# Kernel tuning notes

Measured on AMD Instinct MI355X. Metric: run time of the kernel, lower is better.

## Reference

```python
import jax, jax.numpy as jnp
import numpy as np


def _encode(tab, idx):
    # tab: [F, V, D]; idx: [..., F] int -> sum_f tab[f, idx[..., f]] -> [..., D]
    g = jax.vmap(lambda t, i: t[i], in_axes=(0, -1), out_axes=0)(tab, idx)
    return g.sum(0)


def _diffuse(fea, ei, w, order):
    # fea: [N, D]; ei: [2, E]; w: [E] learned edge weights
    N = fea.shape[0]
    r, c = ei[0], ei[1]
    adj = jnp.zeros((N, N), fea.dtype).at[r, c].set(w).at[c, r].set(w)
    adj = adj + jnp.eye(N, dtype=fea.dtype)
    r_col_inv = adj.sum(1) ** -0.5  # from degree over axis 1
    r_row_inv = adj.sum(0) ** -0.5  # from degree over axis 0
    A = r_row_inv[:, None] * adj * r_col_inv[None, :]
    x = fea
    y = fea
    for _ in range(order):
        x = jax.lax.stop_gradient(A @ x)
        y = y + x
    return jax.lax.stop_gradient(y / (order + 1.0))


def setup_inputs():
    B, N, E, EMB, L, FA, FB, V = 512, 128, 512, 300, 5, 9, 3, 64
    k = jax.random.split(jax.random.key(0), 12)
    s = 0.02
    return {
        "order": 3,
        "x_atom": jax.random.randint(k[0], (B, N, FA), 0, V),
        "edge_index": jax.random.randint(k[1], (B, 2, E), 0, N),
        "edge_attr": jax.random.randint(k[2], (B, E, FB), 0, V),
        "atom_tab": jax.random.normal(k[3], (FA, V, EMB)) * s,
        "bond_tab_root": jax.random.normal(k[4], (FB, V, EMB)) * s,
        "edge_lin_w": jax.random.normal(k[5], (EMB,)) * s,
        "edge_lin_b": jnp.zeros(()),
        "bond_tabs": jax.random.normal(k[6], (L, FB, V, EMB)) * s,
        "eps": jnp.zeros((L,)),
        "w1": jax.random.normal(k[7], (L, EMB, 2 * EMB)) * s,
        "b1": jnp.zeros((L, 2 * EMB)),
        "bn1_g": jnp.ones((L, 2 * EMB)),
        "bn1_b": jnp.zeros((L, 2 * EMB)),
        "w2": jax.random.normal(k[8], (L, 2 * EMB, EMB)) * s,
        "b2": jnp.zeros((L, EMB)),
        "bn_g": jnp.ones((L, EMB)),
        "bn_b": jnp.zeros((L, EMB)),
    }


def reference(order, x_atom, edge_index, edge_attr, atom_tab, bond_tab_root,
              edge_lin_w, edge_lin_b, bond_tabs, eps, w1, b1, bn1_g, bn1_b,
              w2, b2, bn_g, bn_b):
    B, N = x_atom.shape[:2]
    E = edge_index.shape[-1]
    L = w1.shape[0]
    DROP = 0.2  # node-feature drop rate (eval-mode scaling)

    # --- per-graph dense-adjacency diffusion (vmapped over graphs) ---
    fea = _encode(atom_tab, x_atom) * (1.0 - DROP)                 # [B, N, D]
    e_emb = _encode(bond_tab_root, edge_attr)                      # [B, E, D]
    ew = jax.nn.sigmoid(e_emb @ edge_lin_w + edge_lin_b)           # [B, E]
    h = jax.vmap(_diffuse, in_axes=(0, 0, 0, None))(fea, edge_index, ew, order)
    h = h.reshape(B * N, -1)                                       # [B*N, D]

    # --- globally-batched GIN message passing ---
    off = (jnp.arange(B) * N)[:, None]
    src = (edge_index[:, 0, :] + off).reshape(-1)                  # [B*E]
    dst = (edge_index[:, 1, :] + off).reshape(-1)
    ea_flat = edge_attr.reshape(B * E, -1)

    for l in range(L):
        ee = _encode(bond_tabs[l], ea_flat)                        # [B*E, D]
        msg = jax.nn.relu(h[src] + ee)
        agg = jax.ops.segment_sum(msg, dst, num_segments=B * N)
        z = (1.0 + eps[l]) * h + agg
        z = z @ w1[l] + b1[l]
        z = bn1_g[l] * z + bn1_b[l]   # eval-mode BN (running mean 0, var 1)
        z = jax.nn.relu(z)
        z = z @ w2[l] + b2[l]
        z = bn_g[l] * z + bn_b[l]     # outer eval-mode BN
        if l < L - 1:
            z = jax.nn.relu(z)
        h = z
    return h
```

## Files before the change

kernel.cpp:

```cpp
#include <hip/hip_runtime.h>

#define NGRAPH 512
#define NNODE  128
#define NEDGE  512
#define EMB    300
#define NLAYER 5
#define FA     9
#define FB     3
#define VV     64
#define KPAD   136

typedef __bf16 bf16x8 __attribute__((ext_vector_type(8)));
typedef __bf16 bf16x4 __attribute__((ext_vector_type(4)));
typedef float  f32x4  __attribute__((ext_vector_type(4)));

__device__ __forceinline__ void gload_lds16(const void* gptr, void* lptr) {
    __builtin_amdgcn_global_load_lds(
        (const __attribute__((address_space(1))) void*)gptr,
        (__attribute__((address_space(3))) void*)lptr, 16, 0, 0);
}

__global__ __launch_bounds__(256)
void prep_w_kernel(const float* __restrict__ w1, const float* __restrict__ w2,
                   __bf16* __restrict__ w1t, __bf16* __restrict__ w2t)
{
    const int i = blockIdx.x * 256 + threadIdx.x;
    const int T1 = NLAYER * 640 * 320;
    const int T2 = NLAYER * 320 * 640;
    if (i < T1) {
        const int l = i / (640 * 320);
        const int r = i - l * 640 * 320;
        const int n = r / 320, k = r - n * 320;
        float v = (n < 600 && k < 300) ? w1[((size_t)l * 300 + k) * 600 + n] : 0.f;
        w1t[i] = (__bf16)v;
    } else if (i < T1 + T2) {
        const int j = i - T1;
        const int l = j / (320 * 640);
        const int r = j - l * 320 * 640;
        const int n = r / 640, k = r - n * 640;
        float v = (n < 300 && k < 600) ? w2[((size_t)l * 600 + k) * 300 + n] : 0.f;
        w2t[j] = (__bf16)v;
    }
}

__global__ __launch_bounds__(512)
void adj_kernel(const int* __restrict__ edge_index,
                const int* __restrict__ edge_attr,
                const float* __restrict__ bond_tab_root,
                const float* __restrict__ edge_lin_w,
                const float* __restrict__ edge_lin_b,
                __bf16* __restrict__ Ahi_g, __bf16* __restrict__ Alo_g)
{
    __shared__ float A[128 * 129];
    __shared__ float ew_s[NEDGE];
    __shared__ int   es[NEDGE];
    __shared__ float rinv[128];
    __shared__ float cinv[128];

    const int tid = threadIdx.x;
    const int g   = blockIdx.x;
    int* Ai = (int*)A;

    for (int e = tid; e < NEDGE; e += 512) {
        int r = edge_index[(g * 2 + 0) * NEDGE + e];
        int c = edge_index[(g * 2 + 1) * NEDGE + e];
        es[e] = r | (c << 8);
    }
    for (int i = tid; i < 128 * 129; i += 512) Ai[i] = -1;
    __syncthreads();

    {
        const int wave = tid >> 6, lane = tid & 63;
        const float elb = edge_lin_b[0];
        for (int e = wave * 64; e < wave * 64 + 64; ++e) {
            const int base = (g * NEDGE + e) * 3;
            const int a0 = edge_attr[base + 0];
            const int a1 = edge_attr[base + 1];
            const int a2 = edge_attr[base + 2];
            const float* t0 = bond_tab_root + (0 * VV + a0) * EMB;
            const float* t1 = bond_tab_root + (1 * VV + a1) * EMB;
            const float* t2 = bond_tab_root + (2 * VV + a2) * EMB;
            float acc = 0.f;
            for (int d = lane; d < EMB; d += 64)
                acc += (t0[d] + t1[d] + t2[d]) * edge_lin_w[d];
            #pragma unroll
            for (int off = 32; off > 0; off >>= 1) acc += __shfl_xor(acc, off, 64);
            if (lane == 0) ew_s[e] = 1.f / (1.f + expf(-(acc + elb)));
        }
    }
    for (int e = tid; e < NEDGE; e += 512) {
        int r = es[e] & 255, c = es[e] >> 8;
        atomicMax(&Ai[r * 129 + c], e);
        atomicMax(&Ai[c * 129 + r], 512 + e);
    }
    __syncthreads();
    for (int i = tid; i < 128 * 129; i += 512) {
        int p = Ai[i];
        A[i] = (p < 0) ? 0.f : ew_s[p & 511];
    }
    __syncthreads();
    if (tid < 128) A[tid * 129 + tid] += 1.f;
    __syncthreads();
    if (tid < 128) {
        float rs = 0.f, cs = 0.f;
        for (int j = 0; j < 128; ++j) { rs += A[tid * 129 + j]; cs += A[j * 129 + tid]; }
        rinv[tid] = 1.f / sqrtf(rs);
        cinv[tid] = 1.f / sqrtf(cs);
    }
    __syncthreads();
    for (int i = tid; i < 128 * KPAD; i += 512) {
        const int m = i / KPAD, k = i - m * KPAD;
        float v = (k < 128) ? A[m * 129 + k] * cinv[m] * rinv[k] : 0.f;
        __bf16 hi = (__bf16)v;
        Ahi_g[(size_t)g * 128 * KPAD + i] = hi;
        Alo_g[(size_t)g * 128 * KPAD + i] = (__bf16)(v - (float)hi);
    }
}

__global__ __launch_bounds__(512)
void diffuse_mm_kernel(const int* __restrict__ order_p,
                       const int* __restrict__ x_atom,
                       const float* __restrict__ atom_tab,
                       const __bf16* __restrict__ Ahi_g,
                       const __bf16* __restrict__ Alo_g,
                       float* __restrict__ h)
{
    __shared__ __bf16 Ahi[128 * KPAD];
    __shared__ __bf16 Alo[128 * KPAD];
    __shared__ __bf16 xt[4 * 64 * KPAD];
    __shared__ int    xat[128 * FA];

    const int tid  = threadIdx.x;
    const int g    = blockIdx.x;
    const int lane = tid & 63;
    const int wid  = tid >> 6;
    const int wm   = (wid >> 1) * 32;
    const int wn   = (wid & 1) * 32;
    const int lr   = lane & 15;
    const int q4   = (lane >> 4) * 4;
    const int kc   = (lane >> 4) * 8;

    for (int idx = tid; idx < 128 * KPAD / 8; idx += 512) {
        gload_lds16(Ahi_g + (size_t)g * 128 * KPAD + idx * 8, (char*)Ahi + idx * 16);
        gload_lds16(Alo_g + (size_t)g * 128 * KPAD + idx * 8, (char*)Alo + idx * 16);
    }
    for (int i = tid; i < 128 * FA; i += 512) xat[i] = x_atom[g * 128 * FA + i];
    __syncthreads();

    const int   ord    = order_p[0];
    const float yscale = 1.f / (float)(ord + 1);

    for (int cb = 0; cb < 5; ++cb) {
        const int dbase = cb * 64;

        float yacc[2][2][4];
        #pragma unroll
        for (int mi = 0; mi < 2; ++mi) {
            #pragma unroll
            for (int ni = 0; ni < 2; ++ni) {
                const int n_ = wn + ni * 16 + lr;
                const int d  = dbase + n_;
                #pragma unroll
                for (int r = 0; r < 4; ++r) {
                    const int m_ = wm + mi * 16 + q4 + r;
                    float v = 0.f;
                    if (d < EMB) {
                        #pragma unroll
                        for (int f = 0; f < FA; ++f)
                            v += atom_tab[(size_t)((f << 6) + xat[m_ * FA + f]) * EMB + d];
                        v *= 0.8f;
                    }
                    yacc[mi][ni][r] = v;
                    __bf16 hi = (__bf16)v;
                    xt[0 * 64 * KPAD + n_ * KPAD + m_] = hi;
                    xt[1 * 64 * KPAD + n_ * KPAD + m_] = (__bf16)(v - (float)hi);
                }
            }
        }
        __syncthreads();

        int curbuf = 0;
        for (int o = 0; o < ord; ++o) {
            const __bf16* xh = xt + (curbuf * 2 + 0) * 64 * KPAD;
            const __bf16* xl = xt + (curbuf * 2 + 1) * 64 * KPAD;
            f32x4 racc[2][2];
            #pragma unroll
            for (int mi = 0; mi < 2; ++mi)
                #pragma unroll
                for (int ni = 0; ni < 2; ++ni) racc[mi][ni] = (f32x4){0.f, 0.f, 0.f, 0.f};

            #pragma unroll
            for (int ks = 0; ks < 4; ++ks) {
                const int k0 = ks * 32 + kc;
                bf16x8 ah[2], al[2], bh[2], bl[2];
                #pragma unroll
                for (int mi = 0; mi < 2; ++mi) {
                    ah[mi] = *(const bf16x8*)&Ahi[(wm + mi * 16 + lr) * KPAD + k0];
                    al[mi] = *(const bf16x8*)&Alo[(wm + mi * 16 + lr) * KPAD + k0];
                }
                #pragma unroll
                for (int ni = 0; ni < 2; ++ni) {
                    bh[ni] = *(const bf16x8*)&xh[(wn + ni * 16 + lr) * KPAD + k0];
                    bl[ni] = *(const bf16x8*)&xl[(wn + ni * 16 + lr) * KPAD + k0];
                }
                #pragma unroll
                for (int mi = 0; mi < 2; ++mi) {
                    #pragma unroll
                    for (int ni = 0; ni < 2; ++ni) {
                        racc[mi][ni] = __builtin_amdgcn_mfma_f32_16x16x32_bf16(
                            ah[mi], bh[ni], racc[mi][ni], 0, 0, 0);
                        racc[mi][ni] = __builtin_amdgcn_mfma_f32_16x16x32_bf16(
                            ah[mi], bl[ni], racc[mi][ni], 0, 0, 0);
                        racc[mi][ni] = __builtin_amdgcn_mfma_f32_16x16x32_bf16(
                            al[mi], bh[ni], racc[mi][ni], 0, 0, 0);
                    }
                }
            }

            __bf16* nh = xt + ((curbuf ^ 1) * 2 + 0) * 64 * KPAD;
            __bf16* nl = xt + ((curbuf ^ 1) * 2 + 1) * 64 * KPAD;
            #pragma unroll
            for (int mi = 0; mi < 2; ++mi) {
                #pragma unroll
                for (int ni = 0; ni < 2; ++ni) {
                    const int n_ = wn + ni * 16 + lr;
                    const int mbase = wm + mi * 16 + q4;
                    bf16x4 hv, lv;
                    #pragma unroll
                    for (int r = 0; r < 4; ++r) {
                        const float v = racc[mi][ni][r];
                        yacc[mi][ni][r] += v;
                        __bf16 hi = (__bf16)v;
                        hv[r] = hi;
                        lv[r] = (__bf16)(v - (float)hi);
                    }
                    *(bf16x4*)&nh[n_ * KPAD + mbase] = hv;
                    *(bf16x4*)&nl[n_ * KPAD + mbase] = lv;
                }
            }
            __syncthreads();
            curbuf ^= 1;
        }

        #pragma unroll
        for (int mi = 0; mi < 2; ++mi) {
            #pragma unroll
            for (int ni = 0; ni < 2; ++ni) {
                const int n_ = wn + ni * 16 + lr;
                const int d  = dbase + n_;
                if (d < EMB) {
                    #pragma unroll
                    for (int r = 0; r < 4; ++r) {
                        const int m_ = wm + mi * 16 + q4 + r;
                        h[(size_t)(g * 128 + m_) * EMB + d] = yacc[mi][ni][r] * yscale;
                    }
                }
            }
        }
    }
}

__global__ __launch_bounds__(1024)
void agg_kernel(const int* __restrict__ edge_index,
                const int* __restrict__ edge_attr,
                const float* __restrict__ bond_tabs,
                const float* __restrict__ eps_all,
                const int l,
                const float* __restrict__ h,
                __bf16* __restrict__ zb)
{
    __shared__ __bf16         hs[128 * 160];
    __shared__ int            epk[NEDGE];
    __shared__ unsigned short eord[NEDGE];
    __shared__ int            cnt[128];
    __shared__ int            off_[129];
    __shared__ int            fill[128];

    const int tid  = threadIdx.x;
    const int g    = blockIdx.x >> 1;
    const int coff = (blockIdx.x & 1) * 160;
    const int wave = tid >> 6, lane = tid & 63;
    const float epl = 1.f + eps_all[l];
    const float* bt = bond_tabs + (size_t)l * FB * VV * EMB;

    if (tid < 128) { cnt[tid] = 0; fill[tid] = 0; }
    __syncthreads();
    if (tid < NEDGE) {
        const int s_ = edge_index[(g * 2 + 0) * NEDGE + tid];
        const int d_ = edge_index[(g * 2 + 1) * NEDGE + tid];
        const int base = (g * NEDGE + tid) * 3;
        epk[tid] = s_ | (d_ << 7) | (edge_attr[base + 0] << 14)
                 | (edge_attr[base + 1] << 20) | (edge_attr[base + 2] << 26);
        atomicAdd(&cnt[d_], 1);
    }
    for (int idx = tid; idx < 128 * 40; idx += 1024) {
        const int r = idx / 40, q = (idx - r * 40) * 4;
        bf16x4 v;
        #pragma unroll
        for (int j = 0; j < 4; ++j) {
            const int d = coff + q + j;
            v[j] = (__bf16)((d < EMB) ? h[(size_t)(g * 128 + r) * EMB + d] : 0.f);
        }
        *(bf16x4*)&hs[r * 160 + q] = v;
    }
    __syncthreads();
    if (tid < 64) {
        const int a = cnt[tid];
        const int b = cnt[64 + tid];
        int ia = a;
        #pragma unroll
        for (int o = 1; o < 64; o <<= 1) {
            int t = __shfl_up(ia, o, 64);
            if (tid >= o) ia += t;
        }
        const int totA = __shfl(ia, 63, 64);
        int ib = b;
        #pragma unroll
        for (int o = 1; o < 64; o <<= 1) {
            int t = __shfl_up(ib, o, 64);
            if (tid >= o) ib += t;
        }
        off_[tid]      = ia - a;
        off_[64 + tid] = totA + ib - b;
        if (tid == 63) off_[128] = totA + ib;
    }
    __syncthreads();
    if (tid < NEDGE) {
        const int d_ = (epk[tid] >> 7) & 127;
        const int pos = off_[d_] + atomicAdd(&fill[d_], 1);
        eord[pos] = (unsigned short)tid;
    }
    __syncthreads();

    const int d0 = lane, d1 = lane + 64, d2 = lane + 128;
    const bool r0 = (coff + d0) < EMB;
    const bool r1 = (coff + d1) < EMB;
    const bool r2 = (d2 < 160) && ((coff + d2) < EMB);

    for (int n = wave; n < 128; n += 16) {
        const float* hrow = h + (size_t)(g * 128 + n) * EMB + coff;
        float a0 = r0 ? epl * hrow[d0] : 0.f;
        float a1 = r1 ? epl * hrow[d1] : 0.f;
        float a2 = r2 ? epl * hrow[d2] : 0.f;
        const int eEnd = off_[n + 1];
        for (int ee = off_[n]; ee < eEnd; ++ee) {
            const int p   = epk[eord[ee]];
            const int src = p & 127;
            const float* t0 = bt + ((p >> 14) & 63) * EMB + coff;
            const float* t1 = bt + (64  + ((p >> 20) & 63)) * EMB + coff;
            const float* t2 = bt + (128 + ((p >> 26) & 63)) * EMB + coff;
            if (r0) a0 += fmaxf((float)hs[src * 160 + d0] + t0[d0] + t1[d0] + t2[d0], 0.f);
            if (r1) a1 += fmaxf((float)hs[src * 160 + d1] + t0[d1] + t1[d1] + t2[d1], 0.f);
            if (r2) a2 += fmaxf((float)hs[src * 160 + d2] + t0[d2] + t1[d2] + t2[d2], 0.f);
        }
        __bf16* zrow = zb + (size_t)(g * 128 + n) * 320 + coff;
        zrow[d0] = (__bf16)a0;
        zrow[d1] = (__bf16)a1;
        if (d2 < 160) zrow[d2] = (__bf16)a2;
    }
}

template <int ABF16, int CBF16, int RELU>
__global__ __launch_bounds__(256)
void gemm_mfma(const void* __restrict__ Av, const int lda, const int Kreal,
               const int nT, const int nBlkN, const __bf16* __restrict__ B,
               void* __restrict__ Cv, const int ldc, const int Nreal,
               const float* __restrict__ bias, const float* __restrict__ gam,
               const float* __restrict__ bet)
{
    __shared__ unsigned short As[128 * 32];
    __shared__ unsigned short Bs[64 * 32];

    const int tid  = threadIdx.x;
    const int nwg  = gridDim.x;
    const int hw   = blockIdx.x;
    const int lg   = (hw & 7) * (nwg >> 3) + (hw >> 3);
    const int bn   = (lg % nBlkN) * 64;
    const int bm   = (lg / nBlkN) * 128;
    const int wid  = tid >> 6;
    const int lane = tid & 63;
    const int wm   = (wid >> 1) * 64;
    const int wn   = (wid & 1) * 32;
    const int lr   = lane & 15;
    const int kc   = (lane >> 4) * 8;
    const int KP   = nT * 32;

    f32x4 acc[4][2];
    #pragma unroll
    for (int mi = 0; mi < 4; ++mi)
        #pragma unroll
        for (int ni = 0; ni < 2; ++ni) acc[mi][ni] = (f32x4){0.f, 0.f, 0.f, 0.f};

    for (int t = 0; t < nT; ++t) {
        const int k0 = t * 32;
        {
            const int n = tid >> 2, k8 = (tid & 3) * 8;
            gload_lds16(B + (size_t)(bn + n) * KP + k0 + k8,
                        (char*)Bs + tid * 16);
        }
        if (ABF16) {
            const __bf16* A = (const __bf16*)Av;
            #pragma unroll
            for (int q = 0; q < 2; ++q) {
                const int idx = q * 256 + tid;
                const int m = idx >> 2, k8 = (idx & 3) * 8;
                gload_lds16(A + (size_t)(bm + m) * lda + k0 + k8,
                            (char*)As + idx * 16);
            }
        } else {
            const float* A = (const float*)Av;
            #pragma unroll
            for (int q = 0; q < 2; ++q) {
                const int idx = q * 256 + tid;
                const int m = idx >> 2;
                const int k = k0 + (idx & 3) * 8;
                const float* src = A + (size_t)(bm + m) * lda + k;
                float v[8];
                if (k + 7 < Kreal) {
                    const float4 u0 = *(const float4*)src;
                    const float4 u1 = *(const float4*)(src + 4);
                    v[0] = u0.x; v[1] = u0.y; v[2] = u0.z; v[3] = u0.w;
                    v[4] = u1.x; v[5] = u1.y; v[6] = u1.z; v[7] = u1.w;
                } else {
                    #pragma unroll
                    for (int j = 0; j < 8; ++j) v[j] = (k + j < Kreal) ? src[j] : 0.f;
                }
                bf16x8 p;
                #pragma unroll
                for (int j = 0; j < 8; ++j) p[j] = (__bf16)v[j];
                *(bf16x8*)&As[idx * 8] = p;
            }
        }
        __syncthreads();

        bf16x8 a[4], bfr[2];
        #pragma unroll
        for (int mi = 0; mi < 4; ++mi)
            a[mi] = *(const bf16x8*)&As[(wm + mi * 16 + lr) * 32 + kc];
        #pragma unroll
        for (int ni = 0; ni < 2; ++ni)
            bfr[ni] = *(const bf16x8*)&Bs[(wn + ni * 16 + lr) * 32 + kc];
        #pragma unroll
        for (int mi = 0; mi < 4; ++mi)
            #pragma unroll
            for (int ni = 0; ni < 2; ++ni)
                acc[mi][ni] = __builtin_amdgcn_mfma_f32_16x16x32_bf16(
                    a[mi], bfr[ni], acc[mi][ni], 0, 0, 0);
        __syncthreads();
    }

    #pragma unroll
    for (int ni = 0; ni < 2; ++ni) {
        const int n = bn + wn + ni * 16 + lr;
        const bool nv = (n < Nreal);
        const float gv = nv ? gam[n]  : 0.f;
        const float bv = nv ? bias[n] : 0.f;
        const float ev = nv ? bet[n]  : 0.f;
        #pragma unroll
        for (int mi = 0; mi < 4; ++mi) {
            #pragma unroll
            for (int r = 0; r < 4; ++r) {
                const size_t m = bm + wm + mi * 16 + (lane >> 4) * 4 + r;
                float v = gv * (acc[mi][ni][r] + bv) + ev;
                if (RELU) v = fmaxf(v, 0.f);
                if (CBF16) {
                    ((__bf16*)Cv)[m * ldc + n] = (__bf16)v;
                } else if (nv) {
                    ((float*)Cv)[m * ldc + n] = v;
                }
            }
        }
    }
}

extern "C" void kernel_launch(void* const* d_in, const int* in_sizes, int n_in,
                              void* d_out, int out_size, void* d_ws, size_t ws_size,
                              hipStream_t stream)
{
    const int*   order_p       = (const int*)d_in[0];
    const int*   x_atom        = (const int*)d_in[1];
    const int*   edge_index    = (const int*)d_in[2];
    const int*   edge_attr     = (const int*)d_in[3];
    const float* atom_tab      = (const float*)d_in[4];
    const float* bond_tab_root = (const float*)d_in[5];
    const float* edge_lin_w    = (const float*)d_in[6];
    const float* edge_lin_b    = (const float*)d_in[7];
    const float* bond_tabs     = (const float*)d_in[8];
    const float* eps           = (const float*)d_in[9];
    const float* w1            = (const float*)d_in[10];
    const float* b1            = (const float*)d_in[11];
    const float* bn1g          = (const float*)d_in[12];
    const float* bn1b          = (const float*)d_in[13];
    const float* w2            = (const float*)d_in[14];
    const float* b2            = (const float*)d_in[15];
    const float* bng           = (const float*)d_in[16];
    const float* bnb           = (const float*)d_in[17];

    float* h = (float*)d_out;

    char* ws = (char*)d_ws;
    __bf16* Ahi_g = (__bf16*)ws;
    __bf16* Alo_g = (__bf16*)(ws + 17825792);
    __bf16* z1    = (__bf16*)ws;
    __bf16* w1t   = (__bf16*)(ws + 83886080);
    __bf16* w2t   = (__bf16*)(ws + 83886080 + 2048000);
    __bf16* zb    = (__bf16*)(ws + 83886080 + 4096000);

    prep_w_kernel<<<8000, 256, 0, stream>>>(w1, w2, w1t, w2t);

    adj_kernel<<<NGRAPH, 512, 0, stream>>>(edge_index, edge_attr, bond_tab_root,
                                           edge_lin_w, edge_lin_b, Ahi_g, Alo_g);

    diffuse_mm_kernel<<<NGRAPH, 512, 0, stream>>>(order_p, x_atom, atom_tab,
                                                  Ahi_g, Alo_g, h);

    for (int l = 0; l < NLAYER; ++l) {
        agg_kernel<<<NGRAPH * 2, 1024, 0, stream>>>(
            edge_index, edge_attr, bond_tabs, eps, l, h, zb);

        gemm_mfma<1, 1, 1><<<5120, 256, 0, stream>>>(
            zb, 320, 320, 10, 10, w1t + (size_t)l * 640 * 320,
            z1, 640, 600, b1 + l * 600, bn1g + l * 600, bn1b + l * 600);

        if (l < NLAYER - 1) {
            gemm_mfma<1, 0, 1><<<2560, 256, 0, stream>>>(
                z1, 640, 640, 20, 5, w2t + (size_t)l * 320 * 640,
                h, EMB, 300, b2 + l * 300, bng + l * 300, bnb + l * 300);
        } else {
            gemm_mfma<1, 0, 0><<<2560, 256, 0, stream>>>(
                z1, 640, 640, 20, 5, w2t + (size_t)l * 320 * 640,
                h, EMB, 300, b2 + l * 300, bng + l * 300, bnb + l * 300);
        }
    }
}
```

Baseline: 1.176 ms.

## Precompute per-graph CSR once and keep intermediate node features in padded bf16

Adds a csr_kernel that builds the destination-sorted packed edge list and offsets once per graph, so the five agg_kernel launches no longer rebuild them with atomics and scans each layer. The diffusion output and the intermediate second-GEMM outputs are now stored as bf16 rows padded to 320 in the output buffer, and agg loads them with vector copies instead of converting from fp32. This halves the node-feature traffic and removes per-layer setup. It adds one extra launch, and the csr kernel's serial scan over 512 edges per thread is slow but runs only once.

Measured after the change: 1.097 ms. 6.7% less time.

```diff
diff --git a/kernel.cpp b/kernel.cpp
--- a/kernel.cpp
+++ b/kernel.cpp
@@ -43,6 +43,60 @@
     }
 }
 
+__global__ __launch_bounds__(128)
+void csr_kernel(const int* __restrict__ edge_index,
+                const int* __restrict__ edge_attr,
+                int* __restrict__ epk_sorted,
+                int* __restrict__ off_g)
+{
+    __shared__ int epk_s[NEDGE];
+    __shared__ int cnt[128];
+    __shared__ int off_[129];
+
+    const int tid = threadIdx.x;
+    const int g   = blockIdx.x;
+
+    cnt[tid] = 0;
+    __syncthreads();
+    for (int e = tid; e < NEDGE; e += 128) {
+        const int s_ = edge_index[(g * 2 + 0) * NEDGE + e];
+        const int d_ = edge_index[(g * 2 + 1) * NEDGE + e];
+        const int base = (g * NEDGE + e) * 3;
+        epk_s[e] = s_ | (d_ << 7) | (edge_attr[base + 0] << 14)
+                 | (edge_attr[base + 1] << 20) | (edge_attr[base + 2] << 26);
+        atomicAdd(&cnt[d_], 1);
+    }
+    __syncthreads();
+    if (tid < 64) {
+        const int a = cnt[tid];
+        const int b = cnt[64 + tid];
+        int ia = a;
+        #pragma unroll
+        for (int o = 1; o < 64; o <<= 1) {
+            int t = __shfl_up(ia, o, 64);
+            if (tid >= o) ia += t;
+        }
+        const int totA = __shfl(ia, 63, 64);
+        int ib = b;
+        #pragma unroll
+        for (int o = 1; o < 64; o <<= 1) {
+            int t = __shfl_up(ib, o, 64);
+            if (tid >= o) ib += t;
+        }
+        off_[tid]      = ia - a;
+        off_[64 + tid] = totA + ib - b;
+        if (tid == 63) off_[128] = totA + ib;
+    }
+    __syncthreads();
+    off_g[g * 129 + tid] = off_[tid];
+    if (tid == 0) off_g[g * 129 + 128] = off_[128];
+    int pos = off_[tid];
+    for (int e = 0; e < NEDGE; ++e) {
+        const int p = epk_s[e];
+        if (((p >> 7) & 127) == tid) epk_sorted[(g << 9) + pos++] = p;
+    }
+}
+
 __global__ __launch_bounds__(512)
 void adj_kernel(const int* __restrict__ edge_index,
                 const int* __restrict__ edge_attr,
@@ -123,7 +177,7 @@
                        const float* __restrict__ atom_tab,
                        const __bf16* __restrict__ Ahi_g,
                        const __bf16* __restrict__ Alo_g,
-                       float* __restrict__ h)
+                       __bf16* __restrict__ hb)
 {
     __shared__ __bf16 Ahi[128 * KPAD];
     __shared__ __bf16 Alo[128 * KPAD];
@@ -248,12 +302,11 @@
             for (int ni = 0; ni < 2; ++ni) {
                 const int n_ = wn + ni * 16 + lr;
                 const int d  = dbase + n_;
-                if (d < EMB) {
-                    #pragma unroll
-                    for (int r = 0; r < 4; ++r) {
-                        const int m_ = wm + mi * 16 + q4 + r;
-                        h[(size_t)(g * 128 + m_) * EMB + d] = yacc[mi][ni][r] * yscale;
-                    }
+                #pragma unroll
+                for (int r = 0; r < 4; ++r) {
+                    const int m_ = wm + mi * 16 + q4 + r;
+                    const float v = (d < EMB) ? yacc[mi][ni][r] * yscale : 0.f;
+                    hb[(size_t)(g * 128 + m_) * 320 + d] = (__bf16)v;
                 }
             }
         }
@@ -261,20 +314,15 @@
 }
 
 __global__ __launch_bounds__(1024)
-void agg_kernel(const int* __restrict__ edge_index,
-                const int* __restrict__ edge_attr,
+void agg_kernel(const __bf16* __restrict__ hb,
+                const int* __restrict__ epk_sorted,
+                const int* __restrict__ off_g,
                 const float* __restrict__ bond_tabs,
                 const float* __restrict__ eps_all,
                 const int l,
-                const float* __restrict__ h,
                 __bf16* __restrict__ zb)
 {
-    __shared__ __bf16         hs[128 * 160];
-    __shared__ int            epk[NEDGE];
-    __shared__ unsigned short eord[NEDGE];
-    __shared__ int            cnt[128];
-    __shared__ int            off_[129];
-    __shared__ int            fill[128];
+    __shared__ __bf16 hs[128 * 160];
 
     const int tid  = threadIdx.x;
     const int g    = blockIdx.x >> 1;
@@ -283,52 +331,10 @@
     const float epl = 1.f + eps_all[l];
     const float* bt = bond_tabs + (size_t)l * FB * VV * EMB;
 
-    if (tid < 128) { cnt[tid] = 0; fill[tid] = 0; }
-    __syncthreads();
-    if (tid < NEDGE) {
-        const int s_ = edge_index[(g * 2 + 0) * NEDGE + tid];
-        const int d_ = edge_index[(g * 2 + 1) * NEDGE + tid];
-        const int base = (g * NEDGE + tid) * 3;
-        epk[tid] = s_ | (d_ << 7) | (edge_attr[base + 0] << 14)
-                 | (edge_attr[base + 1] << 20) | (edge_attr[base + 2] << 26);
-        atomicAdd(&cnt[d_], 1);
-    }
-    for (int idx = tid; idx < 128 * 40; idx += 1024) {
-        const int r = idx / 40, q = (idx - r * 40) * 4;
-        bf16x4 v;
-        #pragma unroll
-        for (int j = 0; j < 4; ++j) {
-            const int d = coff + q + j;
-            v[j] = (__bf16)((d < EMB) ? h[(size_t)(g * 128 + r) * EMB + d] : 0.f);
-        }
-        *(bf16x4*)&hs[r * 160 + q] = v;
-    }
-    __syncthreads();
-    if (tid < 64) {
-        const int a = cnt[tid];
-        const int b = cnt[64 + tid];
-        int ia = a;
-        #pragma unroll
-        for (int o = 1; o < 64; o <<= 1) {
-            int t = __shfl_up(ia, o, 64);
-            if (tid >= o) ia += t;
-        }
-        const int totA = __shfl(ia, 63, 64);
-        int ib = b;
-        #pragma unroll
-        for (int o = 1; o < 64; o <<= 1) {
-            int t = __shfl_up(ib, o, 64);
-            if (tid >= o) ib += t;
-        }
-        off_[tid]      = ia - a;
-        off_[64 + tid] = totA + ib - b;
-        if (tid == 63) off_[128] = totA + ib;
-    }
-    __syncthreads();
-    if (tid < NEDGE) {
-        const int d_ = (epk[tid] >> 7) & 127;
-        const int pos = off_[d_] + atomicAdd(&fill[d_], 1);
-        eord[pos] = (unsigned short)tid;
+    for (int idx = tid; idx < 128 * 20; idx += 1024) {
+        const int r = idx / 20, c = idx - r * 20;
+        *(bf16x8*)&hs[r * 160 + c * 8] =
+            *(const bf16x8*)&hb[(size_t)(g * 128 + r) * 320 + coff + c * 8];
     }
     __syncthreads();
 
@@ -337,14 +343,16 @@
     const bool r1 = (coff + d1) < EMB;
     const bool r2 = (d2 < 160) && ((coff + d2) < EMB);
 
+    const int* offg = off_g + g * 129;
+    const int* epkg = epk_sorted + (g << 9);
+
     for (int n = wave; n < 128; n += 16) {
-        const float* hrow = h + (size_t)(g * 128 + n) * EMB + coff;
-        float a0 = r0 ? epl * hrow[d0] : 0.f;
-        float a1 = r1 ? epl * hrow[d1] : 0.f;
-        float a2 = r2 ? epl * hrow[d2] : 0.f;
-        const int eEnd = off_[n + 1];
-        for (int ee = off_[n]; ee < eEnd; ++ee) {
-            const int p   = epk[eord[ee]];
+        float a0 = r0 ? epl * (float)hs[n * 160 + d0] : 0.f;
+        float a1 = r1 ? epl * (float)hs[n * 160 + d1] : 0.f;
+        float a2 = r2 ? epl * (float)hs[n * 160 + d2] : 0.f;
+        const int eBeg = offg[n], eEnd = offg[n + 1];
+        for (int ee = eBeg; ee < eEnd; ++ee) {
+            const int p   = epkg[ee];
             const int src = p & 127;
             const float* t0 = bt + ((p >> 14) & 63) * EMB + coff;
             const float* t1 = bt + (64  + ((p >> 20) & 63)) * EMB + coff;
@@ -496,7 +504,8 @@
     const float* bng           = (const float*)d_in[16];
     const float* bnb           = (const float*)d_in[17];
 
-    float* h = (float*)d_out;
+    float*  h  = (float*)d_out;
+    __bf16* hb = (__bf16*)d_out;
 
     char* ws = (char*)d_ws;
     __bf16* Ahi_g = (__bf16*)ws;
@@ -505,27 +514,31 @@
     __bf16* w1t   = (__bf16*)(ws + 83886080);
     __bf16* w2t   = (__bf16*)(ws + 83886080 + 2048000);
     __bf16* zb    = (__bf16*)(ws + 83886080 + 4096000);
+    int*    epk_s = (int*)(ws + 83886080 + 4096000 + 41943040);
+    int*    off_g = (int*)(ws + 83886080 + 4096000 + 41943040 + 1048576);
 
     prep_w_kernel<<<8000, 256, 0, stream>>>(w1, w2, w1t, w2t);
+
+    csr_kernel<<<NGRAPH, 128, 0, stream>>>(edge_index, edge_attr, epk_s, off_g);
 
     adj_kernel<<<NGRAPH, 512, 0, stream>>>(edge_index, edge_attr, bond_tab_root,
                                            edge_lin_w, edge_lin_b, Ahi_g, Alo_g);
 
     diffuse_mm_kernel<<<NGRAPH, 512, 0, stream>>>(order_p, x_atom, atom_tab,
-                                                  Ahi_g, Alo_g, h);
+                                                  Ahi_g, Alo_g, hb);
 
     for (int l = 0; l < NLAYER; ++l) {
         agg_kernel<<<NGRAPH * 2, 1024, 0, stream>>>(
-            edge_index, edge_attr, bond_tabs, eps, l, h, zb);
+            hb, epk_s, off_g, bond_tabs, eps, l, zb);
 
         gemm_mfma<1, 1, 1><<<5120, 256, 0, stream>>>(
             zb, 320, 320, 10, 10, w1t + (size_t)l * 640 * 320,
             z1, 640, 600, b1 + l * 600, bn1g + l * 600, bn1b + l * 600);
 
         if (l < NLAYER - 1) {
-            gemm_mfma<1, 0, 1><<<2560, 256, 0, stream>>>(
+            gemm_mfma<1, 1, 1><<<2560, 256, 0, stream>>>(
                 z1, 640, 640, 20, 5, w2t + (size_t)l * 320 * 640,
-                h, EMB, 300, b2 + l * 300, bng + l * 300, bnb + l * 300);
+                hb, 320, 300, b2 + l * 300, bng + l * 300, bnb + l * 300);
         } else {
             gemm_mfma<1, 0, 0><<<2560, 256, 0, stream>>>(
                 z1, 640, 640, 20, 5, w2t + (size_t)l * 320 * 640,
```
